# Kernel optimization log

Measured on AMD Instinct MI355X. Metric: run time of the kernel, lower is better.

Reference implementation:

```python
import jax, jax.numpy as jnp
import numpy as np

EMBED = 512
HEADS = 8
HD = EMBED // HEADS


def setup_inputs() -> dict:
    key = jax.random.key(0)
    ks = jax.random.split(key, 8)
    N, L = 4, 2048
    queries = jax.random.normal(ks[0], (N, L, EMBED), dtype=jnp.float32)
    keys = jax.random.normal(ks[1], (N, L, EMBED), dtype=jnp.float32)
    values = jax.random.normal(ks[2], (N, L, EMBED), dtype=jnp.float32)
    s = 1.0 / np.sqrt(HD)
    Wq = jax.random.normal(ks[3], (HD, HD), dtype=jnp.float32) * s
    Wk = jax.random.normal(ks[4], (HD, HD), dtype=jnp.float32) * s
    Wv = jax.random.normal(ks[5], (HD, HD), dtype=jnp.float32) * s
    Wo = jax.random.normal(ks[6], (EMBED, EMBED), dtype=jnp.float32) * (1.0 / np.sqrt(EMBED))
    bo = jax.random.normal(ks[7], (EMBED,), dtype=jnp.float32) * 0.01
    return {"queries": queries, "keys": keys, "values": values,
            "Wq": Wq, "Wk": Wk, "Wv": Wv, "Wo": Wo, "bo": bo}


def reference(queries, keys, values, Wq, Wk, Wv, Wo, bo):
    N, Lq, _ = queries.shape
    Lk = keys.shape[1]
    # split heads: [N, L, H, D]
    q = queries.reshape(N, Lq, HEADS, HD)
    k = keys.reshape(N, Lk, HEADS, HD)
    v = values.reshape(N, Lk, HEADS, HD)
    # per-head linear projections (weights shared across heads); torch Linear: x @ W.T
    q = jnp.einsum('nqhd,ed->nqhe', q, Wq)
    k = jnp.einsum('nkhd,ed->nkhe', k, Wk)
    v = jnp.einsum('nkhd,ed->nkhe', v, Wv)
    # scores scaled by sqrt(embed_size) (as in the original, NOT sqrt(head_dim))
    energy = jnp.einsum('nqhd,nkhd->nhqk', q, k) / jnp.sqrt(jnp.float32(EMBED))
    attn = jax.nn.softmax(energy, axis=-1)
    out = jnp.einsum('nhqk,nkhd->nqhd', attn, v).reshape(N, Lq, EMBED)
    return out @ Wo.T + bo
```

## Files before the change

### kernel.cpp

```cpp
#include <hip/hip_runtime.h>
#include <math.h>

#define N_ 4
#define L_ 2048
#define E_ 512
#define H_ 8
#define D_ 64

#define QSCALE 0.06375871588055019f

typedef short s16x8 __attribute__((ext_vector_type(8)));
typedef float f32x4 __attribute__((ext_vector_type(4)));
typedef float f32x16 __attribute__((ext_vector_type(16)));
typedef unsigned int u32x4 __attribute__((ext_vector_type(4)));

typedef const __attribute__((address_space(1))) unsigned int ga_u32;
typedef __attribute__((address_space(3))) unsigned int lds_u32;

__device__ __forceinline__ void gl_lds16(const unsigned short* g, unsigned short* l) {
    __builtin_amdgcn_global_load_lds((ga_u32*)g, (lds_u32*)l, 16, 0, 0);
}
__device__ __forceinline__ float exp2a(float x) {
    float r; asm("v_exp_f32 %0, %1" : "=v"(r) : "v"(x)); return r;
}
__device__ __forceinline__ unsigned int cvtpk(float lo, float hi) {
    unsigned int r; asm("v_cvt_pk_bf16_f32 %0, %1, %2" : "=v"(r) : "v"(lo), "v"(hi)); return r;
}
__device__ __forceinline__ void swap32(unsigned int& a, unsigned int& b) {
    asm volatile("v_permlane32_swap_b32 %0, %1" : "+v"(a), "+v"(b));
}
__device__ __forceinline__ float max3f(float a, float b, float c) {
    return fmaxf(fmaxf(a, b), c);
}
__device__ __forceinline__ unsigned short f2bf(float x) {
    unsigned int u = __builtin_bit_cast(unsigned int, x);
    u = (u + 0x7FFFu + ((u >> 16) & 1u)) >> 16;
    return (unsigned short)u;
}
__device__ __forceinline__ float bflo(unsigned int w) {
    return __builtin_bit_cast(float, w << 16);
}
__device__ __forceinline__ float bfhi(unsigned int w) {
    return __builtin_bit_cast(float, w & 0xFFFF0000u);
}
__device__ __forceinline__ s16x8 ld8(const unsigned short* p) {
    return *reinterpret_cast<const s16x8*>(p);
}

__global__ __launch_bounds__(256) void wo_split_kernel(
    const float* __restrict__ Wo, unsigned short* __restrict__ Whi,
    unsigned short* __restrict__ Wlo)
{
    const int i = blockIdx.x * 256 + threadIdx.x;
    const float4 w = reinterpret_cast<const float4*>(Wo)[i];
    const unsigned int hxy = cvtpk(w.x, w.y);
    const unsigned int hzw = cvtpk(w.z, w.w);
    const unsigned int lxy = cvtpk(w.x - bflo(hxy), w.y - bfhi(hxy));
    const unsigned int lzw = cvtpk(w.z - bflo(hzw), w.w - bfhi(hzw));
    uint2 hh; hh.x = hxy; hh.y = hzw;
    uint2 ll; ll.x = lxy; ll.y = lzw;
    reinterpret_cast<uint2*>(Whi)[i] = hh;
    reinterpret_cast<uint2*>(Wlo)[i] = ll;
}

__global__ __launch_bounds__(256) void qkv_proj_kernel(
    const float* __restrict__ Q, const float* __restrict__ K, const float* __restrict__ V,
    const float* __restrict__ Wq, const float* __restrict__ Wk, const float* __restrict__ Wv,
    unsigned short* __restrict__ Qp, unsigned short* __restrict__ Kp,
    unsigned short* __restrict__ Vt)
{
    __shared__ __align__(16) unsigned short Xl[4096];
    __shared__ __align__(16) unsigned short Whl[4096];
    __shared__ __align__(16) unsigned short Wll[4096];
    __shared__ __align__(16) unsigned short Yl[64][72];

    const int tid = threadIdx.x;
    const int lt = blockIdx.x;
    const int nh = blockIdx.y;
    const int m  = blockIdx.z;
    const int n = nh >> 3, h = nh & 7;
    const int l0 = lt * 64;

    const float* __restrict__ in = (m == 0) ? Q : (m == 1) ? K : V;
    const float* __restrict__ W  = (m == 0) ? Wq : (m == 1) ? Wk : Wv;

    const int xr = tid >> 2;
    const int xc = (tid & 3) * 16;
    {
        const float* xs = in + (size_t)(n * L_ + l0 + xr) * E_ + h * D_ + xc;
        float4 a = reinterpret_cast<const float4*>(xs)[0];
        float4 b = reinterpret_cast<const float4*>(xs)[1];
        float4 c = reinterpret_cast<const float4*>(xs)[2];
        float4 d = reinterpret_cast<const float4*>(xs)[3];
        u32x4 w0, w1;
        w0[0] = cvtpk(a.x, a.y); w0[1] = cvtpk(a.z, a.w);
        w0[2] = cvtpk(b.x, b.y); w0[3] = cvtpk(b.z, b.w);
        w1[0] = cvtpk(c.x, c.y); w1[1] = cvtpk(c.z, c.w);
        w1[2] = cvtpk(d.x, d.y); w1[3] = cvtpk(d.z, d.w);
        const int base  = (xr * 64 + xc) ^ ((xr & 7) << 3);
        const int base2 = (xr * 64 + xc + 8) ^ ((xr & 7) << 3);
        *reinterpret_cast<u32x4*>(&Xl[base])  = w0;
        *reinterpret_cast<u32x4*>(&Xl[base2]) = w1;

        const float* wsrc = W + (size_t)xr * D_ + xc;
        float wv[16];
#pragma unroll
        for (int i = 0; i < 4; ++i) {
            const float4 t = reinterpret_cast<const float4*>(wsrc)[i];
            wv[i * 4 + 0] = t.x; wv[i * 4 + 1] = t.y;
            wv[i * 4 + 2] = t.z; wv[i * 4 + 3] = t.w;
        }
        if (m == 0) {
#pragma unroll
            for (int i = 0; i < 16; ++i) wv[i] *= QSCALE;
        }
        u32x4 hi0, hi1, lo0, lo1;
#pragma unroll
        for (int i = 0; i < 4; ++i) {
            const unsigned int hw = cvtpk(wv[2 * i], wv[2 * i + 1]);
            hi0[i] = hw;
            lo0[i] = cvtpk(wv[2 * i] - bflo(hw), wv[2 * i + 1] - bfhi(hw));
        }
#pragma unroll
        for (int i = 0; i < 4; ++i) {
            const unsigned int hw = cvtpk(wv[8 + 2 * i], wv[8 + 2 * i + 1]);
            hi1[i] = hw;
            lo1[i] = cvtpk(wv[8 + 2 * i] - bflo(hw), wv[8 + 2 * i + 1] - bfhi(hw));
        }
        *reinterpret_cast<u32x4*>(&Whl[base])  = hi0;
        *reinterpret_cast<u32x4*>(&Whl[base2]) = hi1;
        *reinterpret_cast<u32x4*>(&Wll[base])  = lo0;
        *reinterpret_cast<u32x4*>(&Wll[base2]) = lo1;
    }
    __syncthreads();

    const int wave = tid >> 6, lane = tid & 63;
    const int ql = lane & 15, g = lane >> 4;
    const int arow = wave * 16 + ql;

    f32x4 acc[4];
#pragma unroll
    for (int t = 0; t < 4; ++t) acc[t] = (f32x4){0.f, 0.f, 0.f, 0.f};

    if (m < 2) {
        s16x8 xf[2];
#pragma unroll
        for (int ks = 0; ks < 2; ++ks)
            xf[ks] = ld8(&Xl[(arow * 64 + ks * 32 + g * 8) ^ ((arow & 7) << 3)]);
#pragma unroll
        for (int t = 0; t < 4; ++t) {
            const int wrow = t * 16 + ql;
#pragma unroll
            for (int ks = 0; ks < 2; ++ks) {
                const s16x8 bh = ld8(&Whl[(wrow * 64 + ks * 32 + g * 8) ^ ((wrow & 7) << 3)]);
                acc[t] = __builtin_amdgcn_mfma_f32_16x16x32_bf16(xf[ks], bh, acc[t], 0, 0, 0);
                const s16x8 bl = ld8(&Wll[(wrow * 64 + ks * 32 + g * 8) ^ ((wrow & 7) << 3)]);
                acc[t] = __builtin_amdgcn_mfma_f32_16x16x32_bf16(xf[ks], bl, acc[t], 0, 0, 0);
            }
        }
    } else {
        s16x8 whf[2], wlf[2];
#pragma unroll
        for (int ks = 0; ks < 2; ++ks) {
            whf[ks] = ld8(&Whl[(arow * 64 + ks * 32 + g * 8) ^ ((arow & 7) << 3)]);
            wlf[ks] = ld8(&Wll[(arow * 64 + ks * 32 + g * 8) ^ ((arow & 7) << 3)]);
        }
#pragma unroll
        for (int t = 0; t < 4; ++t) {
            const int xrow = t * 16 + ql;
#pragma unroll
            for (int ks = 0; ks < 2; ++ks) {
                const s16x8 bx = ld8(&Xl[(xrow * 64 + ks * 32 + g * 8) ^ ((xrow & 7) << 3)]);
                acc[t] = __builtin_amdgcn_mfma_f32_16x16x32_bf16(whf[ks], bx, acc[t], 0, 0, 0);
                acc[t] = __builtin_amdgcn_mfma_f32_16x16x32_bf16(wlf[ks], bx, acc[t], 0, 0, 0);
            }
        }
    }

#pragma unroll
    for (int t = 0; t < 4; ++t)
#pragma unroll
        for (int r = 0; r < 4; ++r)
            Yl[wave * 16 + g * 4 + r][t * 16 + ql] = f2bf(acc[t][r]);
    __syncthreads();

    const int orow = tid >> 2;
    const int oc = (tid & 3) * 16;
    const uint4 v0 = *reinterpret_cast<const uint4*>(&Yl[orow][oc]);
    const uint4 v1 = *reinterpret_cast<const uint4*>(&Yl[orow][oc + 8]);
    unsigned short* dst;
    if (m == 0)      dst = Qp + ((size_t)nh * L_ + l0 + orow) * D_ + oc;
    else if (m == 1) dst = Kp + ((size_t)nh * L_ + l0 + orow) * D_ + oc;
    else             dst = Vt + ((size_t)nh * D_ + orow) * L_ + l0 + oc;
    *reinterpret_cast<uint4*>(dst) = v0;
    *reinterpret_cast<uint4*>(dst + 8) = v1;
}

__global__ __launch_bounds__(512, 2) void attn_kernel(
    const unsigned short* __restrict__ Qp, const unsigned short* __restrict__ Kp,
    const unsigned short* __restrict__ Vt, unsigned short* __restrict__ AO)
{
    __shared__ __align__(16) unsigned short ST[2][4 * 4096];

    const int tid = threadIdx.x;
    const int phys = blockIdx.x;
    const int bid = (phys & 7) * 64 + (phys >> 3);
    const int qt = bid & 15;
    const int nh = bid >> 4;
    const int n = nh >> 3, h = nh & 7;
    const int q0 = qt * 128;
    const int wave = tid >> 6;
    const int half = wave >> 2;
    const int w4 = wave & 3;
    const int lane = tid & 63;
    const int l31 = lane & 31;
    const int hh  = lane >> 5;

    const unsigned short* __restrict__ Qb = Qp + (size_t)nh * (L_ * D_);
    const unsigned short* __restrict__ Kb = Kp + (size_t)nh * (L_ * D_);
    const unsigned short* __restrict__ Vb = Vt + (size_t)nh * (D_ * L_);

    unsigned short* const Kbuf0 = &ST[half][0];
    unsigned short* const Kbuf1 = &ST[half][4096];
    unsigned short* const Vbuf0 = &ST[half][2 * 4096];
    unsigned short* const Vbuf1 = &ST[half][3 * 4096];

    const int G0 = w4 * 64 + lane;
    const int G1 = G0 + 256;
    const int r0 = G0 >> 3, c0 = (G0 & 7) ^ (r0 & 7);
    const int r1 = G1 >> 3, c1 = (G1 & 7) ^ (r1 & 7);

    const int kbase = half * 1024;
    const unsigned short* ks0 = Kb + (size_t)(kbase + r0) * 64 + c0 * 8;
    const unsigned short* ks1 = Kb + (size_t)(kbase + r1) * 64 + c1 * 8;
    const unsigned short* vs0 = Vb + (size_t)r0 * L_ + kbase + c0 * 8;
    const unsigned short* vs1 = Vb + (size_t)r1 * L_ + kbase + c1 * 8;

    gl_lds16(ks0, Kbuf0 + w4 * 512);
    gl_lds16(ks1, Kbuf0 + 2048 + w4 * 512);
    gl_lds16(vs0, Vbuf0 + w4 * 512);
    gl_lds16(vs1, Vbuf0 + 2048 + w4 * 512);

    const int qrow = q0 + w4 * 32 + l31;
    s16x8 qfrag[4];
#pragma unroll
    for (int ks = 0; ks < 4; ++ks)
        qfrag[ks] = ld8(Qb + (size_t)qrow * D_ + ks * 16 + hh * 8);

    float m_ = -INFINITY;
    float lsum = 0.f;
    f32x16 ot[2];
    ot[0] = (f32x16)0.f;
    ot[1] = (f32x16)0.f;
    s16x8 pf[4];

    const int NT = (L_ / 2) / 64;

    for (int kt = 0; kt < NT; ++kt) {
        __syncthreads();
        if (kt + 1 < NT) {
            unsigned short* kn = ((kt + 1) & 1) ? Kbuf1 : Kbuf0;
            gl_lds16(ks0 + (kt + 1) * 4096, kn + w4 * 512);
            gl_lds16(ks1 + (kt + 1) * 4096, kn + 2048 + w4 * 512);
        }
        const unsigned short* __restrict__ Kl = (kt & 1) ? Kbuf1 : Kbuf0;
        unsigned short* const vprev = (kt & 1) ? Vbuf0 : Vbuf1;

        f32x16 st[2];
        __builtin_amdgcn_s_setprio(1);
#pragma unroll
        for (int kv = 0; kv < 2; ++kv) {
            st[kv] = (f32x16)0.f;
            const int krow = kv * 32 + l31;
#pragma unroll
            for (int ks = 0; ks < 4; ++ks) {
                const s16x8 kf = ld8(&Kl[(krow * 64 + ks * 16 + hh * 8) ^ ((krow & 7) << 3)]);
                st[kv] = __builtin_amdgcn_mfma_f32_32x32x16_bf16(kf, qfrag[ks], st[kv], 0, 0, 0);
            }
        }

        if (kt) {
#pragma unroll
            for (int dt = 0; dt < 2; ++dt) {
                const int drow = dt * 32 + l31;
#pragma unroll
                for (int kc = 0; kc < 4; ++kc) {
                    const s16x8 vf = ld8(&vprev[(drow * 64 + kc * 16 + hh * 8) ^ ((drow & 7) << 3)]);
                    ot[dt] = __builtin_amdgcn_mfma_f32_32x32x16_bf16(vf, pf[kc], ot[dt], 0, 0, 0);
                }
            }
        }
        __builtin_amdgcn_s_setprio(0);

        __syncthreads();
        if (kt + 1 < NT) {
            gl_lds16(vs0 + (kt + 1) * 64, vprev + w4 * 512);
            gl_lds16(vs1 + (kt + 1) * 64, vprev + 2048 + w4 * 512);
        }

        const float t0 = max3f(st[0][0],  st[0][1],  st[0][2]);
        const float t1 = max3f(st[0][3],  st[0][4],  st[0][5]);
        const float t2 = max3f(st[0][6],  st[0][7],  st[0][8]);
        const float t3 = max3f(st[0][9],  st[0][10], st[0][11]);
        const float t4 = max3f(st[0][12], st[0][13], st[0][14]);
        const float t5 = max3f(st[0][15], st[1][0],  st[1][1]);
        const float t6 = max3f(st[1][2],  st[1][3],  st[1][4]);
        const float t7 = max3f(st[1][5],  st[1][6],  st[1][7]);
        const float t8 = max3f(st[1][8],  st[1][9],  st[1][10]);
        const float t9 = max3f(st[1][11], st[1][12], st[1][13]);
        const float ta = fmaxf(st[1][14], st[1][15]);
        const float u0 = max3f(t0, t1, t2);
        const float u1 = max3f(t3, t4, t5);
        const float u2 = max3f(t6, t7, t8);
        const float u3 = fmaxf(t9, ta);
        float tmax = fmaxf(max3f(u0, u1, u2), u3);
        tmax = fmaxf(tmax, __shfl_xor(tmax, 32));

        if (!__all(tmax <= m_ + 8.f)) {
            const float newm = fmaxf(m_, tmax);
            const float corr = exp2a(m_ - newm);
            lsum *= corr;
            ot[0] *= corr;
            ot[1] *= corr;
            m_ = newm;
        }

#pragma unroll
        for (int kv = 0; kv < 2; ++kv)
#pragma unroll
            for (int i = 0; i < 16; ++i) st[kv][i] = exp2a(st[kv][i] - m_);

        {
            float s0 = 0.f, s1 = 0.f, s2 = 0.f, s3 = 0.f;
#pragma unroll
            for (int i = 0; i < 4; ++i) {
                s0 += st[0][i];      s1 += st[0][i + 4];
                s2 += st[0][i + 8];  s3 += st[0][i + 12];
                s0 += st[1][i];      s1 += st[1][i + 4];
                s2 += st[1][i + 8];  s3 += st[1][i + 12];
            }
            float ts = (s0 + s1) + (s2 + s3);
            ts += __shfl_xor(ts, 32);
            lsum += ts;
        }

#pragma unroll
        for (int kv = 0; kv < 2; ++kv) {
            unsigned int A0 = cvtpk(st[kv][0],  st[kv][1]),  B0 = cvtpk(st[kv][2],  st[kv][3]);
            unsigned int A1 = cvtpk(st[kv][4],  st[kv][5]),  B1 = cvtpk(st[kv][6],  st[kv][7]);
            unsigned int A2 = cvtpk(st[kv][8],  st[kv][9]),  B2 = cvtpk(st[kv][10], st[kv][11]);
            unsigned int A3 = cvtpk(st[kv][12], st[kv][13]), B3 = cvtpk(st[kv][14], st[kv][15]);
            swap32(A0, A1); swap32(B0, B1);
            swap32(A2, A3); swap32(B2, B3);
            u32x4 lo; lo[0] = A0; lo[1] = B0; lo[2] = A1; lo[3] = B1;
            u32x4 hi; hi[0] = A2; hi[1] = B2; hi[2] = A3; hi[3] = B3;
            pf[kv * 2 + 0] = __builtin_bit_cast(s16x8, lo);
            pf[kv * 2 + 1] = __builtin_bit_cast(s16x8, hi);
        }
    }

    unsigned short* const vlast = ((NT - 1) & 1) ? Vbuf1 : Vbuf0;
    __builtin_amdgcn_s_setprio(1);
#pragma unroll
    for (int dt = 0; dt < 2; ++dt) {
        const int drow = dt * 32 + l31;
#pragma unroll
        for (int kc = 0; kc < 4; ++kc) {
            const s16x8 vf = ld8(&vlast[(drow * 64 + kc * 16 + hh * 8) ^ ((drow & 7) << 3)]);
            ot[dt] = __builtin_amdgcn_mfma_f32_32x32x16_bf16(vf, pf[kc], ot[dt], 0, 0, 0);
        }
    }
    __builtin_amdgcn_s_setprio(0);

    __syncthreads();
    float* mrg = reinterpret_cast<float*>(&ST[0][0]);
    const int slot = ((w4 << 6) + lane) * 36;
    if (half == 1) {
        *reinterpret_cast<f32x16*>(&mrg[slot])      = ot[0];
        *reinterpret_cast<f32x16*>(&mrg[slot + 16]) = ot[1];
        mrg[slot + 32] = m_;
        mrg[slot + 33] = lsum;
    }
    __syncthreads();
    if (half == 0) {
        const f32x16 ob0 = *reinterpret_cast<const f32x16*>(&mrg[slot]);
        const f32x16 ob1 = *reinterpret_cast<const f32x16*>(&mrg[slot + 16]);
        const float mB = mrg[slot + 32];
        const float lB = mrg[slot + 33];
        const float mm = fmaxf(m_, mB);
        const float sA = exp2a(m_ - mm);
        const float sB = exp2a(mB - mm);
        const float inv = 1.f / (lsum * sA + lB * sB);
        ot[0] = ot[0] * sA + ob0 * sB;
        ot[1] = ot[1] * sA + ob1 * sB;

#pragma unroll
        for (int dt = 0; dt < 2; ++dt) {
#pragma unroll
            for (int r = 0; r < 4; ++r) {
                uint2 o;
                o.x = cvtpk(ot[dt][4 * r + 0] * inv, ot[dt][4 * r + 1] * inv);
                o.y = cvtpk(ot[dt][4 * r + 2] * inv, ot[dt][4 * r + 3] * inv);
                const size_t elem = ((size_t)n * L_ + qrow) * E_ + h * D_ + dt * 32 + r * 8 + hh * 4;
                *reinterpret_cast<uint2*>(AO + elem) = o;
            }
        }
    }
}

__global__ __launch_bounds__(256) void out_proj_kernel(
    const unsigned short* __restrict__ AO, const unsigned short* __restrict__ Whi,
    const unsigned short* __restrict__ Wlo, const float* __restrict__ bo,
    float* __restrict__ out)
{
    __shared__ __align__(16) unsigned short Adb[2][4096];
    __shared__ __align__(16) unsigned short Hdb[2][4096];
    __shared__ __align__(16) unsigned short Ldb[2][4096];

    const int tid = threadIdx.x;
    const int bid = blockIdx.x;
    const int mt = bid >> 3, nt = bid & 7;
    const int m0 = mt * 64, n0 = nt * 64;
    const int wave = tid >> 6, lane = tid & 63;
    const int ql = lane & 15, g = lane >> 4;

    const int G0 = wave * 64 + lane;
    const int G1 = G0 + 256;
    const int r0 = G0 >> 3, c0 = (G0 & 7) ^ (r0 & 7);
    const int r1 = G1 >> 3, c1 = (G1 & 7) ^ (r1 & 7);

    const unsigned short* as0 = AO + (size_t)(m0 + r0) * E_ + c0 * 8;
    const unsigned short* as1 = AO + (size_t)(m0 + r1) * E_ + c1 * 8;
    const unsigned short* hs0 = Whi + (size_t)(n0 + r0) * E_ + c0 * 8;
    const unsigned short* hs1 = Whi + (size_t)(n0 + r1) * E_ + c1 * 8;
    const unsigned short* ls0 = Wlo + (size_t)(n0 + r0) * E_ + c0 * 8;
    const unsigned short* ls1 = Wlo + (size_t)(n0 + r1) * E_ + c1 * 8;

    gl_lds16(as0, &Adb[0][wave * 512]);
    gl_lds16(as1, &Adb[0][2048 + wave * 512]);
    gl_lds16(hs0, &Hdb[0][wave * 512]);
    gl_lds16(hs1, &Hdb[0][2048 + wave * 512]);
    gl_lds16(ls0, &Ldb[0][wave * 512]);
    gl_lds16(ls1, &Ldb[0][2048 + wave * 512]);

    float bias[4];
#pragma unroll
    for (int t = 0; t < 4; ++t) bias[t] = bo[n0 + t * 16 + ql];

    f32x4 acc[4];
#pragma unroll
    for (int t = 0; t < 4; ++t) acc[t] = (f32x4){0.f, 0.f, 0.f, 0.f};

    const int arow = wave * 16 + ql;

    for (int kc = 0; kc < 8; ++kc) {
        const int b = kc & 1;
        __syncthreads();
        if (kc + 1 < 8) {
            const int nb = b ^ 1;
            const int ko = (kc + 1) * 64;
            gl_lds16(as0 + ko, &Adb[nb][wave * 512]);
            gl_lds16(as1 + ko, &Adb[nb][2048 + wave * 512]);
            gl_lds16(hs0 + ko, &Hdb[nb][wave * 512]);
            gl_lds16(hs1 + ko, &Hdb[nb][2048 + wave * 512]);
            gl_lds16(ls0 + ko, &Ldb[nb][wave * 512]);
            gl_lds16(ls1 + ko, &Ldb[nb][2048 + wave * 512]);
        }
        const unsigned short* __restrict__ Al = Adb[b];
        const unsigned short* __restrict__ Hl = Hdb[b];
        const unsigned short* __restrict__ Ll = Ldb[b];

        s16x8 af[2];
#pragma unroll
        for (int ks = 0; ks < 2; ++ks)
            af[ks] = ld8(&Al[(arow * 64 + ks * 32 + g * 8) ^ ((arow & 7) << 3)]);

        __builtin_amdgcn_s_setprio(1);
#pragma unroll
        for (int t = 0; t < 4; ++t) {
            const int wrow = t * 16 + ql;
#pragma unroll
            for (int ks = 0; ks < 2; ++ks) {
                const s16x8 bh = ld8(&Hl[(wrow * 64 + ks * 32 + g * 8) ^ ((wrow & 7) << 3)]);
                acc[t] = __builtin_amdgcn_mfma_f32_16x16x32_bf16(af[ks], bh, acc[t], 0, 0, 0);
                const s16x8 bl = ld8(&Ll[(wrow * 64 + ks * 32 + g * 8) ^ ((wrow & 7) << 3)]);
                acc[t] = __builtin_amdgcn_mfma_f32_16x16x32_bf16(af[ks], bl, acc[t], 0, 0, 0);
            }
        }
        __builtin_amdgcn_s_setprio(0);
    }

#pragma unroll
    for (int t = 0; t < 4; ++t) {
#pragma unroll
        for (int r = 0; r < 4; ++r) {
            out[(size_t)(m0 + wave * 16 + g * 4 + r) * E_ + n0 + t * 16 + ql] =
                acc[t][r] + bias[t];
        }
    }
}

extern "C" void kernel_launch(void* const* d_in, const int* in_sizes, int n_in,
                              void* d_out, int out_size, void* d_ws, size_t ws_size,
                              hipStream_t stream)
{
    const float* Q  = (const float*)d_in[0];
    const float* K  = (const float*)d_in[1];
    const float* V  = (const float*)d_in[2];
    const float* Wq = (const float*)d_in[3];
    const float* Wk = (const float*)d_in[4];
    const float* Wv = (const float*)d_in[5];
    const float* Wo = (const float*)d_in[6];
    const float* bo = (const float*)d_in[7];
    float* out = (float*)d_out;

    unsigned short* ws = (unsigned short*)d_ws;
    const size_t SZ = (size_t)N_ * H_ * L_ * D_;
    unsigned short* Qp  = ws;
    unsigned short* Kp  = ws + SZ;
    unsigned short* Vt  = ws + 2 * SZ;
    unsigned short* AO  = ws + 3 * SZ;
    unsigned short* Whi = ws + 4 * SZ;
    unsigned short* Wlo = ws + 4 * SZ + 262144;

    qkv_proj_kernel<<<dim3(32, 32, 3), 256, 0, stream>>>(Q, K, V, Wq, Wk, Wv, Qp, Kp, Vt);
    wo_split_kernel<<<256, 256, 0, stream>>>(Wo, Whi, Wlo);
    attn_kernel<<<512, 512, 0, stream>>>(Qp, Kp, Vt, AO);
    out_proj_kernel<<<(8192 / 64) * (E_ / 64), 256, 0, stream>>>(AO, Whi, Wlo, bo, out);
}
```

Before: 94.49 us.

## Split each 64-key attention tile into two 32-key softmax/PV sub-steps

The main attention loop now runs over 32-key sub-steps instead of 64-key tiles. Each step keeps one 32x32 score accumulator and two P fragments instead of two and four. The K/V double-buffer loads and barriers now happen only on even sub-steps, and PV for the previous sub-step reads the matching half of the V tile. This cuts live registers and gives more interleaving between QK and PV MFMAs, in exchange for twice as many max/sum reductions, cross-lane shuffles and rescale checks per key.

```diff
diff --git a/kernel.cpp b/kernel.cpp
--- a/kernel.cpp
+++ b/kernel.cpp
@@ -252,68 +252,68 @@
     f32x16 ot[2];
     ot[0] = (f32x16)0.f;
     ot[1] = (f32x16)0.f;
-    s16x8 pf[4];
-
-    const int NT = (L_ / 2) / 64;
-
-    for (int kt = 0; kt < NT; ++kt) {
-        __syncthreads();
-        if (kt + 1 < NT) {
-            unsigned short* kn = ((kt + 1) & 1) ? Kbuf1 : Kbuf0;
-            gl_lds16(ks0 + (kt + 1) * 4096, kn + w4 * 512);
-            gl_lds16(ks1 + (kt + 1) * 4096, kn + 2048 + w4 * 512);
-        }
-        const unsigned short* __restrict__ Kl = (kt & 1) ? Kbuf1 : Kbuf0;
-        unsigned short* const vprev = (kt & 1) ? Vbuf0 : Vbuf1;
-
-        f32x16 st[2];
+    s16x8 pf[2];
+
+    const int NS = (L_ / 2) / 32;
+
+    for (int s = 0; s < NS; ++s) {
+        const int T = s >> 1;
+        if ((s & 1) == 0) {
+            __syncthreads();
+            if (T + 1 < 16) {
+                unsigned short* kn = ((T + 1) & 1) ? Kbuf1 : Kbuf0;
+                gl_lds16(ks0 + (T + 1) * 4096, kn + w4 * 512);
+                gl_lds16(ks1 + (T + 1) * 4096, kn + 2048 + w4 * 512);
+            }
+        }
+        const unsigned short* __restrict__ Kl = (T & 1) ? Kbuf1 : Kbuf0;
+        const int kro = (s & 1) * 32;
+
+        f32x16 st = (f32x16)0.f;
         __builtin_amdgcn_s_setprio(1);
-#pragma unroll
-        for (int kv = 0; kv < 2; ++kv) {
-            st[kv] = (f32x16)0.f;
-            const int krow = kv * 32 + l31;
+        {
+            const int krow = kro + l31;
+            const int swz = (l31 & 7) << 3;
 #pragma unroll
             for (int ks = 0; ks < 4; ++ks) {
-                const s16x8 kf = ld8(&Kl[(krow * 64 + ks * 16 + hh * 8) ^ ((krow & 7) << 3)]);
-                st[kv] = __builtin_amdgcn_mfma_f32_32x32x16_bf16(kf, qfrag[ks], st[kv], 0, 0, 0);
-            }
-        }
-
-        if (kt) {
+                const s16x8 kf = ld8(&Kl[(krow * 64 + ks * 16 + hh * 8) ^ swz]);
+                st = __builtin_amdgcn_mfma_f32_32x32x16_bf16(kf, qfrag[ks], st, 0, 0, 0);
+            }
+        }
+
+        if (s) {
+            const unsigned short* __restrict__ Vl = (((s - 1) >> 1) & 1) ? Vbuf1 : Vbuf0;
+            const int vco = ((s - 1) & 1) * 32;
 #pragma unroll
             for (int dt = 0; dt < 2; ++dt) {
                 const int drow = dt * 32 + l31;
-#pragma unroll
-                for (int kc = 0; kc < 4; ++kc) {
-                    const s16x8 vf = ld8(&vprev[(drow * 64 + kc * 16 + hh * 8) ^ ((drow & 7) << 3)]);
+                const int swz = (l31 & 7) << 3;
+#pragma unroll
+                for (int kc = 0; kc < 2; ++kc) {
+                    const s16x8 vf = ld8(&Vl[(drow * 64 + vco + kc * 16 + hh * 8) ^ swz]);
                     ot[dt] = __builtin_amdgcn_mfma_f32_32x32x16_bf16(vf, pf[kc], ot[dt], 0, 0, 0);
                 }
             }
         }
         __builtin_amdgcn_s_setprio(0);
 
-        __syncthreads();
-        if (kt + 1 < NT) {
-            gl_lds16(vs0 + (kt + 1) * 64, vprev + w4 * 512);
-            gl_lds16(vs1 + (kt + 1) * 64, vprev + 2048 + w4 * 512);
-        }
-
-        const float t0 = max3f(st[0][0],  st[0][1],  st[0][2]);
-        const float t1 = max3f(st[0][3],  st[0][4],  st[0][5]);
-        const float t2 = max3f(st[0][6],  st[0][7],  st[0][8]);
-        const float t3 = max3f(st[0][9],  st[0][10], st[0][11]);
-        const float t4 = max3f(st[0][12], st[0][13], st[0][14]);
-        const float t5 = max3f(st[0][15], st[1][0],  st[1][1]);
-        const float t6 = max3f(st[1][2],  st[1][3],  st[1][4]);
-        const float t7 = max3f(st[1][5],  st[1][6],  st[1][7]);
-        const float t8 = max3f(st[1][8],  st[1][9],  st[1][10]);
-        const float t9 = max3f(st[1][11], st[1][12], st[1][13]);
-        const float ta = fmaxf(st[1][14], st[1][15]);
+        if ((s & 1) == 0) {
+            __syncthreads();
+            if (T + 1 < 16) {
+                unsigned short* vn = ((T + 1) & 1) ? Vbuf1 : Vbuf0;
+                gl_lds16(vs0 + (T + 1) * 64, vn + w4 * 512);
+                gl_lds16(vs1 + (T + 1) * 64, vn + 2048 + w4 * 512);
+            }
+        }
+
+        const float t0 = max3f(st[0],  st[1],  st[2]);
+        const float t1 = max3f(st[3],  st[4],  st[5]);
+        const float t2 = max3f(st[6],  st[7],  st[8]);
+        const float t3 = max3f(st[9],  st[10], st[11]);
+        const float t4 = max3f(st[12], st[13], st[14]);
         const float u0 = max3f(t0, t1, t2);
-        const float u1 = max3f(t3, t4, t5);
-        const float u2 = max3f(t6, t7, t8);
-        const float u3 = fmaxf(t9, ta);
-        float tmax = fmaxf(max3f(u0, u1, u2), u3);
+        const float u1 = max3f(t3, t4, st[15]);
+        float tmax = fmaxf(u0, u1);
         tmax = fmaxf(tmax, __shfl_xor(tmax, 32));
 
         if (!__all(tmax <= m_ + 8.f)) {
@@ -326,51 +326,50 @@
         }
 
 #pragma unroll
-        for (int kv = 0; kv < 2; ++kv)
-#pragma unroll
-            for (int i = 0; i < 16; ++i) st[kv][i] = exp2a(st[kv][i] - m_);
+        for (int i = 0; i < 16; ++i) st[i] = exp2a(st[i] - m_);
 
         {
             float s0 = 0.f, s1 = 0.f, s2 = 0.f, s3 = 0.f;
 #pragma unroll
             for (int i = 0; i < 4; ++i) {
-                s0 += st[0][i];      s1 += st[0][i + 4];
-                s2 += st[0][i + 8];  s3 += st[0][i + 12];
-                s0 += st[1][i];      s1 += st[1][i + 4];
-                s2 += st[1][i + 8];  s3 += st[1][i + 12];
+                s0 += st[i];      s1 += st[i + 4];
+                s2 += st[i + 8];  s3 += st[i + 12];
             }
             float ts = (s0 + s1) + (s2 + s3);
             ts += __shfl_xor(ts, 32);
             lsum += ts;
         }
 
-#pragma unroll
-        for (int kv = 0; kv < 2; ++kv) {
-            unsigned int A0 = cvtpk(st[kv][0],  st[kv][1]),  B0 = cvtpk(st[kv][2],  st[kv][3]);
-            unsigned int A1 = cvtpk(st[kv][4],  st[kv][5]),  B1 = cvtpk(st[kv][6],  st[kv][7]);
-            unsigned int A2 = cvtpk(st[kv][8],  st[kv][9]),  B2 = cvtpk(st[kv][10], st[kv][11]);
-            unsigned int A3 = cvtpk(st[kv][12], st[kv][13]), B3 = cvtpk(st[kv][14], st[kv][15]);
+        {
+            unsigned int A0 = cvtpk(st[0],  st[1]),  B0 = cvtpk(st[2],  st[3]);
+            unsigned int A1 = cvtpk(st[4],  st[5]),  B1 = cvtpk(st[6],  st[7]);
+            unsigned int A2 = cvtpk(st[8],  st[9]),  B2 = cvtpk(st[10], st[11]);
+            unsigned int A3 = cvtpk(st[12], st[13]), B3 = cvtpk(st[14], st[15]);
             swap32(A0, A1); swap32(B0, B1);
             swap32(A2, A3); swap32(B2, B3);
             u32x4 lo; lo[0] = A0; lo[1] = B0; lo[2] = A1; lo[3] = B1;
             u32x4 hi; hi[0] = A2; hi[1] = B2; hi[2] = A3; hi[3] = B3;
-            pf[kv * 2 + 0] = __builtin_bit_cast(s16x8, lo);
-            pf[kv * 2 + 1] = __builtin_bit_cast(s16x8, hi);
-        }
-    }
-
-    unsigned short* const vlast = ((NT - 1) & 1) ? Vbuf1 : Vbuf0;
-    __builtin_amdgcn_s_setprio(1);
-#pragma unroll
-    for (int dt = 0; dt < 2; ++dt) {
-        const int drow = dt * 32 + l31;
-#pragma unroll
-        for (int kc = 0; kc < 4; ++kc) {
-            const s16x8 vf = ld8(&vlast[(drow * 64 + kc * 16 + hh * 8) ^ ((drow & 7) << 3)]);
-            ot[dt] = __builtin_amdgcn_mfma_f32_32x32x16_bf16(vf, pf[kc], ot[dt], 0, 0, 0);
-        }
-    }
-    __builtin_amdgcn_s_setprio(0);
+            pf[0] = __builtin_bit_cast(s16x8, lo);
+            pf[1] = __builtin_bit_cast(s16x8, hi);
+        }
+    }
+
+    {
+        const unsigned short* __restrict__ Vl = (((NS - 1) >> 1) & 1) ? Vbuf1 : Vbuf0;
+        const int vco = ((NS - 1) & 1) * 32;
+        __builtin_amdgcn_s_setprio(1);
+#pragma unroll
+        for (int dt = 0; dt < 2; ++dt) {
+            const int drow = dt * 32 + l31;
+            const int swz = (l31 & 7) << 3;
+#pragma unroll
+            for (int kc = 0; kc < 2; ++kc) {
+                const s16x8 vf = ld8(&Vl[(drow * 64 + vco + kc * 16 + hh * 8) ^ swz]);
+                ot[dt] = __builtin_amdgcn_mfma_f32_32x32x16_bf16(vf, pf[kc], ot[dt], 0, 0, 0);
+            }
+        }
+        __builtin_amdgcn_s_setprio(0);
+    }
 
     __syncthreads();
     float* mrg = reinterpret_cast<float*>(&ST[0][0]);
```

Result: faster. 91.10 us (-3.6%).
